# Optimization experiments

Measured on AMD Instinct MI355X. Metric: run time of the kernel, lower is better.

Reference implementation:

```python
import jax, jax.numpy as jnp
import numpy as np
import math

D = 1024
L = 4096
B = 4

def setup_inputs() -> dict:
    key = jax.random.key(0)
    ks = jax.random.split(key, 6)
    x = jax.random.normal(ks[0], (B, L, D), dtype=jnp.float32)
    base_phases = jax.random.normal(ks[1], (L, D), dtype=jnp.float32) * math.pi
    s = 1.0 / math.sqrt(D)
    W_v = jax.random.normal(ks[2], (D, D), dtype=jnp.float32) * s
    b_v = jnp.zeros((D,), dtype=jnp.float32)
    ln_g = jnp.ones((D,), dtype=jnp.float32)
    ln_b = jnp.zeros((D,), dtype=jnp.float32)
    W_o = jax.random.normal(ks[3], (D, D), dtype=jnp.float32) * s
    b_o = jnp.zeros((D,), dtype=jnp.float32)
    return {"x": x, "base_phases": base_phases, "W_v": W_v, "b_v": b_v,
            "ln_g": ln_g, "ln_b": ln_b, "W_o": W_o, "b_o": b_o}

def _layernorm(x, g, b, eps=1e-5):
    mu = jnp.mean(x, axis=-1, keepdims=True)
    var = jnp.mean(jnp.square(x - mu), axis=-1, keepdims=True)
    return (x - mu) * jax.lax.rsqrt(var + eps) * g + b

def reference(x, base_phases, W_v, b_v, ln_g, ln_b, W_o, b_o):
    Bv, Lv, Dv = x.shape
    phases = base_phases[:Lv][None, :, :]          # [1, L, D]
    cosp, sinp = jnp.cos(phases), jnp.sin(phases)
    value = jnp.einsum('bld,ed->ble', x, W_v) + b_v  # Linear(D,D)
    mem_real = jnp.cumsum(value * cosp, axis=1)
    mem_imag = jnp.cumsum(value * sinp, axis=1)
    retrieved = (mem_real * cosp + mem_imag * sinp) / math.sqrt(Dv)
    out = jnp.einsum('bld,ed->ble', _layernorm(retrieved, ln_g, ln_b), W_o) + b_o
    return x + out
```

## Files before the change

### kernel.cpp

```cpp
#include <hip/hip_runtime.h>
#include <stdint.h>


#define D_DIM 1024
#define L_DIM 4096
#define B_DIM 4
#define M_DIM (B_DIM * L_DIM)
#define CHUNK 64
#define NCH (L_DIM / CHUNK)
#define NT 16

typedef __attribute__((ext_vector_type(8))) short short8;
typedef __attribute__((ext_vector_type(4))) float f32x4;

__device__ __forceinline__ float bf2f(uint32_t h) {
  union { uint32_t u; float f; } x; x.u = h << 16; return x.f;
}
__device__ __forceinline__ uint16_t f2bf(float f) {
  union { float f; uint32_t u; } x; x.f = f;
  uint32_t u = x.u;
  u += 0x7fffu + ((u >> 16) & 1u);
  return (uint16_t)(u >> 16);
}

__global__ void k_prep(const float* __restrict__ x, const float* __restrict__ Wv,
                       const float* __restrict__ Wo, const float* __restrict__ g,
                       const float* __restrict__ bln, const float* __restrict__ bo,
                       uint16_t* __restrict__ xb, uint16_t* __restrict__ wv,
                       uint16_t* __restrict__ wob, float* __restrict__ u,
                       float* __restrict__ vb) {
  int blk = blockIdx.x;
  int tid = threadIdx.x;
  if (blk < 8192 + 512) {
    const float* in = (blk < 8192) ? x : Wv;
    uint16_t* outp = (blk < 8192) ? xb : wv;
    int base = (blk < 8192) ? blk : (blk - 8192);
    int i = (base * 256 + tid) * 8;
    float4 a = *(const float4*)(in + i);
    float4 b = *(const float4*)(in + i + 4);
    ushort4 o0 = { f2bf(a.x), f2bf(a.y), f2bf(a.z), f2bf(a.w) };
    ushort4 o1 = { f2bf(b.x), f2bf(b.y), f2bf(b.z), f2bf(b.w) };
    *(ushort4*)(outp + i) = o0;
    *(ushort4*)(outp + i + 4) = o1;
    return;
  }
  int e = blk - 8704;
  int d = tid * 4;
  float4 w  = *(const float4*)(Wo + (size_t)e * D_DIM + d);
  float4 gg = *(const float4*)(g + d);
  float4 bb = *(const float4*)(bln + d);
  float gw0 = gg.x * w.x, gw1 = gg.y * w.y, gw2 = gg.z * w.z, gw3 = gg.w * w.w;
  ushort4 o = { f2bf(gw0), f2bf(gw1), f2bf(gw2), f2bf(gw3) };
  *(ushort4*)(wob + (size_t)e * D_DIM + d) = o;
  float su = gw0 + gw1 + gw2 + gw3;
  float sv = bb.x * w.x + bb.y * w.y + bb.z * w.z + bb.w * w.w;
#pragma unroll
  for (int off = 32; off > 0; off >>= 1) {
    su += __shfl_down(su, off);
    sv += __shfl_down(sv, off);
  }
  __shared__ float s1[4], s2[4];
  int wid = tid >> 6, lane = tid & 63;
  if (lane == 0) { s1[wid] = su; s2[wid] = sv; }
  __syncthreads();
  if (tid == 0) {
    u[e]  = s1[0] + s1[1] + s1[2] + s1[3];
    vb[e] = s2[0] + s2[1] + s2[2] + s2[3] + bo[e];
  }
}

template <int MODE>
__global__ __launch_bounds__(512, 2) void k_gemm(
    const uint16_t* __restrict__ A, const uint16_t* __restrict__ W,
    void* __restrict__ outp,
    const float* __restrict__ p0, const float* __restrict__ p1,
    const float* __restrict__ mu, const float* __restrict__ inv,
    const uint16_t* __restrict__ xres) {
  __shared__ char lds[8 * 16384];
  const int tid = threadIdx.x;
  const int lane = tid & 63;
  const int wid = tid >> 6;
  const int wm = wid >> 2;
  const int wn = wid & 3;

  const int idx = blockIdx.x;
  const int bm = (idx & 7) * 8 + ((idx >> 3) >> 2);
  const int bn = (idx >> 3) & 3;

  const int srow = tid >> 3;
  const int scb  = (tid & 7) * 16;
  const int scbs = scb ^ ((srow & 7) << 4);

#define GLL(SRC, DST)                                                            \
  __builtin_amdgcn_global_load_lds((const __attribute__((address_space(1))) void*)(SRC), \
                                   (__attribute__((address_space(3))) void*)(DST), 16, 0, 0)

#define STAGE_A(KS, HA)                                                          \
  do {                                                                           \
    char* _d = lds + ((((KS)&1) * 4 + (HA)) << 14) + tid * 16;                   \
    const char* _s = (const char*)A +                                            \
        (size_t)(bm * 256 + (HA) * 128 + srow) * 2048 + (KS) * 128 + scbs;       \
    GLL(_s, _d);                                                                 \
    GLL(_s + (size_t)64 * 2048, _d + 8192);                                      \
  } while (0)

#define STAGE_B(KS, HB)                                                          \
  do {                                                                           \
    char* _d = lds + ((((KS)&1) * 4 + 2 + (HB)) << 14) + tid * 16;               \
    const char* _s = (const char*)W +                                            \
        (size_t)(bn * 256 + (HB) * 128 + srow) * 2048 + (KS) * 128 + scbs;       \
    GLL(_s, _d);                                                                 \
    GLL(_s + (size_t)64 * 2048, _d + 8192);                                      \
  } while (0)

  const int axor = (lane & 7) << 4;
  const int afr  = lane & 15;
  const int acol = (lane >> 4) * 16;

#define LD_A(PAR, I, KK)                                                         \
  (*(const short8*)(lds + (((PAR) * 4 + wm) << 14) + ((I) * 16 + afr) * 128 +    \
                    (((KK) * 64 + acol) ^ axor)))
#define LD_B(PAR, J, KK)                                                         \
  (*(const short8*)(lds + (((PAR) * 4 + 2 + (wn >> 1)) << 14) +                  \
                    ((wn & 1) * 64 + (J) * 16 + afr) * 128 +                     \
                    (((KK) * 64 + acol) ^ axor)))

#define MFMA(AV, BV, CV) __builtin_amdgcn_mfma_f32_16x16x32_bf16(AV, BV, CV, 0, 0, 0)
#define SB0() __builtin_amdgcn_sched_barrier(0)

  f32x4 acc[8][4];
#pragma unroll
  for (int i = 0; i < 8; ++i)
#pragma unroll
    for (int j = 0; j < 4; ++j)
      acc[i][j] = (f32x4){0.f, 0.f, 0.f, 0.f};

  STAGE_A(0, 0); STAGE_A(0, 1);
  STAGE_B(0, 0); STAGE_B(0, 1);
  asm volatile("s_waitcnt vmcnt(0)" ::: "memory");
  __builtin_amdgcn_s_barrier();

  for (int ks = 0; ks < NT; ++ks) {
    const int par = ks & 1;
    short8 Af0, Af1, Af2, Af3, Bf0, Bf1, Bf2, Bf3;

    Bf0 = LD_B(par, 0, 0); Bf1 = LD_B(par, 1, 0); Bf2 = LD_B(par, 2, 0); Bf3 = LD_B(par, 3, 0);
    Af0 = LD_A(par, 0, 0); Af1 = LD_A(par, 1, 0); Af2 = LD_A(par, 2, 0); Af3 = LD_A(par, 3, 0);
    SB0();
    if (ks + 1 < NT) { STAGE_A(ks + 1, 0); STAGE_A(ks + 1, 1); }
    __builtin_amdgcn_s_barrier();
    asm volatile("s_waitcnt lgkmcnt(0)" ::: "memory");
    SB0();
    __builtin_amdgcn_s_setprio(1);
#pragma unroll
    for (int j = 0; j < 4; ++j) {
      const short8 bj = (j == 0) ? Bf0 : (j == 1) ? Bf1 : (j == 2) ? Bf2 : Bf3;
      acc[0][j] = MFMA(Af0, bj, acc[0][j]);
      acc[1][j] = MFMA(Af1, bj, acc[1][j]);
      acc[2][j] = MFMA(Af2, bj, acc[2][j]);
      acc[3][j] = MFMA(Af3, bj, acc[3][j]);
    }
    __builtin_amdgcn_s_setprio(0);
    __builtin_amdgcn_s_barrier();

    Af0 = LD_A(par, 4, 0); Af1 = LD_A(par, 5, 0); Af2 = LD_A(par, 6, 0); Af3 = LD_A(par, 7, 0);
    SB0();
    if (ks + 1 < NT) { STAGE_B(ks + 1, 0); STAGE_B(ks + 1, 1); }
    __builtin_amdgcn_s_barrier();
    asm volatile("s_waitcnt lgkmcnt(0)" ::: "memory");
    SB0();
    __builtin_amdgcn_s_setprio(1);
#pragma unroll
    for (int j = 0; j < 4; ++j) {
      const short8 bj = (j == 0) ? Bf0 : (j == 1) ? Bf1 : (j == 2) ? Bf2 : Bf3;
      acc[4][j] = MFMA(Af0, bj, acc[4][j]);
      acc[5][j] = MFMA(Af1, bj, acc[5][j]);
      acc[6][j] = MFMA(Af2, bj, acc[6][j]);
      acc[7][j] = MFMA(Af3, bj, acc[7][j]);
    }
    __builtin_amdgcn_s_setprio(0);
    __builtin_amdgcn_s_barrier();

    Bf0 = LD_B(par, 0, 1); Bf1 = LD_B(par, 1, 1); Bf2 = LD_B(par, 2, 1); Bf3 = LD_B(par, 3, 1);
    Af0 = LD_A(par, 0, 1); Af1 = LD_A(par, 1, 1); Af2 = LD_A(par, 2, 1); Af3 = LD_A(par, 3, 1);
    SB0();
    __builtin_amdgcn_s_barrier();
    asm volatile("s_waitcnt lgkmcnt(0)" ::: "memory");
    SB0();
    __builtin_amdgcn_s_setprio(1);
#pragma unroll
    for (int j = 0; j < 4; ++j) {
      const short8 bj = (j == 0) ? Bf0 : (j == 1) ? Bf1 : (j == 2) ? Bf2 : Bf3;
      acc[0][j] = MFMA(Af0, bj, acc[0][j]);
      acc[1][j] = MFMA(Af1, bj, acc[1][j]);
      acc[2][j] = MFMA(Af2, bj, acc[2][j]);
      acc[3][j] = MFMA(Af3, bj, acc[3][j]);
    }
    __builtin_amdgcn_s_setprio(0);
    asm volatile("s_waitcnt vmcnt(4)" ::: "memory");
    __builtin_amdgcn_s_barrier();

    Af0 = LD_A(par, 4, 1); Af1 = LD_A(par, 5, 1); Af2 = LD_A(par, 6, 1); Af3 = LD_A(par, 7, 1);
    SB0();
    __builtin_amdgcn_s_barrier();
    asm volatile("s_waitcnt lgkmcnt(0)" ::: "memory");
    SB0();
    __builtin_amdgcn_s_setprio(1);
#pragma unroll
    for (int j = 0; j < 4; ++j) {
      const short8 bj = (j == 0) ? Bf0 : (j == 1) ? Bf1 : (j == 2) ? Bf2 : Bf3;
      acc[4][j] = MFMA(Af0, bj, acc[4][j]);
      acc[5][j] = MFMA(Af1, bj, acc[5][j]);
      acc[6][j] = MFMA(Af2, bj, acc[6][j]);
      acc[7][j] = MFMA(Af3, bj, acc[7][j]);
    }
    __builtin_amdgcn_s_setprio(0);
    asm volatile("s_waitcnt vmcnt(0)" ::: "memory");
    __builtin_amdgcn_s_barrier();
  }

  if (MODE == 0) {
    uint16_t* outv = (uint16_t*)outp;
    __syncthreads();
#pragma unroll
    for (int i = 0; i < 8; ++i)
#pragma unroll
      for (int r = 0; r < 4; ++r) {
        int row = wm * 128 + i * 16 + (lane >> 4) * 4 + r;
#pragma unroll
        for (int j = 0; j < 4; ++j) {
          int ncol = wn * 64 + j * 16 + (lane & 15);
          float v = acc[i][j][r] + p0[bn * 256 + ncol];
          *(uint16_t*)(lds + row * 512 + ((ncol * 2) ^ ((row & 7) << 4))) = f2bf(v);
        }
      }
    __syncthreads();
    {
      int row = tid >> 1, half = tid & 1;
      uint16_t* gdst = outv + (size_t)(bm * 256 + row) * D_DIM + bn * 256 + half * 128;
#pragma unroll
      for (int s = 0; s < 16; ++s) {
        short8 v = *(const short8*)(lds + row * 512 +
                                    ((half * 256 + s * 16) ^ ((row & 7) << 4)));
        *(short8*)(gdst + s * 8) = v;
      }
    }
  } else {
    float* outf = (float*)outp;
#pragma unroll
    for (int i = 0; i < 8; ++i)
#pragma unroll
      for (int r = 0; r < 4; ++r) {
        int m = bm * 256 + wm * 128 + i * 16 + (lane >> 4) * 4 + r;
        float im = inv[m], mm = mu[m];
#pragma unroll
        for (int j = 0; j < 4; ++j) {
          int n = bn * 256 + wn * 64 + j * 16 + (lane & 15);
          outf[(size_t)m * D_DIM + n] =
              im * acc[i][j][r] - im * mm * p0[n] + p1[n] +
              bf2f(xres[(size_t)m * D_DIM + n]);
        }
      }
  }
#undef GLL
#undef STAGE_A
#undef STAGE_B
#undef LD_A
#undef LD_B
#undef MFMA
#undef SB0
}

__global__ void k_passA(const uint16_t* __restrict__ value, const float* __restrict__ phases,
                        float* __restrict__ pr, float* __restrict__ pi) {
  int d0 = blockIdx.x * 512 + threadIdx.x * 2;
  int c = blockIdx.y, b = blockIdx.z;
  const uint16_t* vp = value + ((size_t)(b * L_DIM + c * CHUNK)) * D_DIM + d0;
  const float* pp = phases + (size_t)(c * CHUNK) * D_DIM + d0;
  float sr0 = 0, si0 = 0, sr1 = 0, si1 = 0;
#pragma unroll 4
  for (int l = 0; l < CHUNK; ++l) {
    uint32_t vv = *(const uint32_t*)vp; vp += D_DIM;
    float2 ph = *(const float2*)pp; pp += D_DIM;
    float v0 = bf2f(vv & 0xffffu), v1 = bf2f(vv >> 16);
    float s0, c0, s1, c1;
    __sincosf(ph.x, &s0, &c0);
    __sincosf(ph.y, &s1, &c1);
    sr0 += v0 * c0; si0 += v0 * s0;
    sr1 += v1 * c1; si1 += v1 * s1;
  }
  size_t o = ((size_t)b * NCH + c) * D_DIM + d0;
  *(float2*)(pr + o) = make_float2(sr0, sr1);
  *(float2*)(pi + o) = make_float2(si0, si1);
}

__global__ void k_passB(float* __restrict__ pr, float* __restrict__ pi) {
  int d = blockIdx.x * 256 + threadIdx.x;
  int b = blockIdx.y;
  size_t base = (size_t)b * NCH * D_DIM + d;
  float r[NCH], im[NCH];
#pragma unroll
  for (int c = 0; c < NCH; ++c) r[c] = pr[base + (size_t)c * D_DIM];
#pragma unroll
  for (int c = 0; c < NCH; ++c) im[c] = pi[base + (size_t)c * D_DIM];
  float rr = 0, ri = 0;
#pragma unroll
  for (int c = 0; c < NCH; ++c) {
    float t = r[c]; r[c] = rr; rr += t;
    t = im[c]; im[c] = ri; ri += t;
  }
#pragma unroll
  for (int c = 0; c < NCH; ++c) pr[base + (size_t)c * D_DIM] = r[c];
#pragma unroll
  for (int c = 0; c < NCH; ++c) pi[base + (size_t)c * D_DIM] = im[c];
}

__global__ void k_passC(const uint16_t* __restrict__ value, const float* __restrict__ phases,
                        const float* __restrict__ pr, const float* __restrict__ pi,
                        uint16_t* __restrict__ ret) {
  int d0 = blockIdx.x * 512 + threadIdx.x * 2;
  int c = blockIdx.y, b = blockIdx.z;
  size_t o = ((size_t)b * NCH + c) * D_DIM + d0;
  float2 r0 = *(const float2*)(pr + o);
  float2 i0 = *(const float2*)(pi + o);
  float mr0 = r0.x, mr1 = r0.y, mi0 = i0.x, mi1 = i0.y;
  size_t rowoff = ((size_t)(b * L_DIM + c * CHUNK)) * D_DIM + d0;
  const uint16_t* vp = value + rowoff;
  uint16_t* rp = ret + rowoff;
  const float* pp = phases + (size_t)(c * CHUNK) * D_DIM + d0;
  const float isd = 0.03125f;
#pragma unroll 4
  for (int l = 0; l < CHUNK; ++l) {
    uint32_t vv = *(const uint32_t*)vp; vp += D_DIM;
    float2 ph = *(const float2*)pp; pp += D_DIM;
    float v0 = bf2f(vv & 0xffffu), v1 = bf2f(vv >> 16);
    float s0, c0, s1, c1;
    __sincosf(ph.x, &s0, &c0);
    __sincosf(ph.y, &s1, &c1);
    mr0 += v0 * c0; mi0 += v0 * s0;
    mr1 += v1 * c1; mi1 += v1 * s1;
    float o0 = (mr0 * c0 + mi0 * s0) * isd;
    float o1 = (mr1 * c1 + mi1 * s1) * isd;
    *(uint32_t*)rp = (uint32_t)f2bf(o0) | ((uint32_t)f2bf(o1) << 16);
    rp += D_DIM;
  }
}

__global__ void k_stats(const uint16_t* __restrict__ ret, float* __restrict__ mu,
                        float* __restrict__ inv) {
  int m = blockIdx.x, tid = threadIdx.x;
  ushort4 v = *(const ushort4*)(ret + (size_t)m * D_DIM + tid * 4);
  float f0 = bf2f(v.x), f1 = bf2f(v.y), f2_ = bf2f(v.z), f3 = bf2f(v.w);
  float s = f0 + f1 + f2_ + f3;
  float ss = f0 * f0 + f1 * f1 + f2_ * f2_ + f3 * f3;
#pragma unroll
  for (int off = 32; off > 0; off >>= 1) {
    s += __shfl_down(s, off);
    ss += __shfl_down(ss, off);
  }
  __shared__ float a1[4], a2[4];
  int wid = tid >> 6, lane = tid & 63;
  if (lane == 0) { a1[wid] = s; a2[wid] = ss; }
  __syncthreads();
  if (tid == 0) {
    float S = a1[0] + a1[1] + a1[2] + a1[3];
    float SS = a2[0] + a2[1] + a2[2] + a2[3];
    float mm = S * (1.0f / 1024.0f);
    float var = SS * (1.0f / 1024.0f) - mm * mm;
    mu[m] = mm;
    inv[m] = rsqrtf(var + 1e-5f);
  }
}

extern "C" void kernel_launch(void* const* d_in, const int* in_sizes, int n_in,
                              void* d_out, int out_size, void* d_ws, size_t ws_size,
                              hipStream_t stream) {
  const float* x      = (const float*)d_in[0];
  const float* phases = (const float*)d_in[1];
  const float* Wv     = (const float*)d_in[2];
  const float* bv     = (const float*)d_in[3];
  const float* lng    = (const float*)d_in[4];
  const float* lnb    = (const float*)d_in[5];
  const float* Wo     = (const float*)d_in[6];
  const float* bo     = (const float*)d_in[7];
  float* out = (float*)d_out;

  char* ws = (char*)d_ws;
  uint16_t* xb    = (uint16_t*)(ws);
  uint16_t* value = (uint16_t*)(ws + (32ull << 20));
  uint16_t* wv    = (uint16_t*)(ws + (64ull << 20));
  uint16_t* wob   = (uint16_t*)(ws + (66ull << 20));
  float* pr       = (float*)(ws + (68ull << 20));
  float* pi       = (float*)(ws + (69ull << 20));
  float* u        = (float*)(ws + (70ull << 20));
  float* vb       = (float*)(ws + (70ull << 20) + 4096);
  float* mu       = (float*)(ws + (71ull << 20));
  float* inv      = (float*)(ws + (72ull << 20));
  uint16_t* retr  = value;

  k_prep<<<8192 + 512 + 1024, 256, 0, stream>>>(x, Wv, Wo, lng, lnb, bo,
                                                xb, wv, wob, u, vb);
  k_gemm<0><<<(M_DIM / 256) * (D_DIM / 256), 512, 0, stream>>>(
      xb, wv, value, bv, nullptr, nullptr, nullptr, nullptr);
  k_passA<<<dim3(2, NCH, B_DIM), 256, 0, stream>>>(value, phases, pr, pi);
  k_passB<<<dim3(D_DIM / 256, B_DIM), 256, 0, stream>>>(pr, pi);
  k_passC<<<dim3(2, NCH, B_DIM), 256, 0, stream>>>(value, phases, pr, pi, retr);
  k_stats<<<M_DIM, 256, 0, stream>>>(retr, mu, inv);
  k_gemm<1><<<(M_DIM / 256) * (D_DIM / 256), 512, 0, stream>>>(
      retr, wob, out, u, vb, mu, inv, xb);
}
```

Before: 149.6 us.

## Fuse fp32-to-bf16 conversion of x into first GEMM's A-tile loading

Removes the separate pass that converted x to a bf16 copy. The first GEMM now loads fp32 x tiles into registers, converts them to bf16 and writes them into swizzled LDS between MFMA phases. The residual add in the output GEMM reads fp32 x directly instead of the bf16 copy, which also slightly improves accuracy. This removes a 64MB read plus 32MB write plus 32MB reread of x, at the cost of double the A-tile global bytes in GEMM0, more registers, and losing the asynchronous global-to-LDS path for A.

```diff
diff --git a/kernel.cpp b/kernel.cpp
--- a/kernel.cpp
+++ b/kernel.cpp
@@ -22,29 +22,28 @@
   u += 0x7fffu + ((u >> 16) & 1u);
   return (uint16_t)(u >> 16);
 }
-
-__global__ void k_prep(const float* __restrict__ x, const float* __restrict__ Wv,
-                       const float* __restrict__ Wo, const float* __restrict__ g,
-                       const float* __restrict__ bln, const float* __restrict__ bo,
-                       uint16_t* __restrict__ xb, uint16_t* __restrict__ wv,
+__device__ __forceinline__ uint32_t pk2(float lo, float hi) {
+  return (uint32_t)f2bf(lo) | ((uint32_t)f2bf(hi) << 16);
+}
+
+__global__ void k_prep(const float* __restrict__ Wv, const float* __restrict__ Wo,
+                       const float* __restrict__ g, const float* __restrict__ bln,
+                       const float* __restrict__ bo, uint16_t* __restrict__ wv,
                        uint16_t* __restrict__ wob, float* __restrict__ u,
                        float* __restrict__ vb) {
   int blk = blockIdx.x;
   int tid = threadIdx.x;
-  if (blk < 8192 + 512) {
-    const float* in = (blk < 8192) ? x : Wv;
-    uint16_t* outp = (blk < 8192) ? xb : wv;
-    int base = (blk < 8192) ? blk : (blk - 8192);
-    int i = (base * 256 + tid) * 8;
-    float4 a = *(const float4*)(in + i);
-    float4 b = *(const float4*)(in + i + 4);
+  if (blk < 512) {
+    int i = (blk * 256 + tid) * 8;
+    float4 a = *(const float4*)(Wv + i);
+    float4 b = *(const float4*)(Wv + i + 4);
     ushort4 o0 = { f2bf(a.x), f2bf(a.y), f2bf(a.z), f2bf(a.w) };
     ushort4 o1 = { f2bf(b.x), f2bf(b.y), f2bf(b.z), f2bf(b.w) };
-    *(ushort4*)(outp + i) = o0;
-    *(ushort4*)(outp + i + 4) = o1;
+    *(ushort4*)(wv + i) = o0;
+    *(ushort4*)(wv + i + 4) = o1;
     return;
   }
-  int e = blk - 8704;
+  int e = blk - 512;
   int d = tid * 4;
   float4 w  = *(const float4*)(Wo + (size_t)e * D_DIM + d);
   float4 gg = *(const float4*)(g + d);
@@ -75,7 +74,7 @@
     void* __restrict__ outp,
     const float* __restrict__ p0, const float* __restrict__ p1,
     const float* __restrict__ mu, const float* __restrict__ inv,
-    const uint16_t* __restrict__ xres) {
+    const float* __restrict__ xres, const float* __restrict__ Af32) {
   __shared__ char lds[8 * 16384];
   const int tid = threadIdx.x;
   const int lane = tid & 63;
@@ -90,6 +89,11 @@
   const int srow = tid >> 3;
   const int scb  = (tid & 7) * 16;
   const int scbs = scb ^ ((srow & 7) << 4);
+
+  const int arow = tid >> 2;
+  const int acf  = (tid & 3) * 16;
+  const int acb  = (tid & 3) * 32;
+  const int aswz = (arow & 7) << 4;
 
 #define GLL(SRC, DST)                                                            \
   __builtin_amdgcn_global_load_lds((const __attribute__((address_space(1))) void*)(SRC), \
@@ -113,6 +117,33 @@
     GLL(_s + (size_t)64 * 2048, _d + 8192);                                      \
   } while (0)
 
+#define A_ISSUE(KS, HA, R)                                                       \
+  do {                                                                           \
+    const float* _s = Af32 + (size_t)(bm * 256 + (HA) * 128 + arow) * D_DIM +    \
+                      (KS) * 64 + acf;                                           \
+    R[0] = *(const float4*)(_s);      R[1] = *(const float4*)(_s + 4);           \
+    R[2] = *(const float4*)(_s + 8);  R[3] = *(const float4*)(_s + 12);          \
+  } while (0)
+
+#define CVT_WRITE(KSP, R0, R1)                                                   \
+  do {                                                                           \
+    char* _d0 = lds + (((KSP) * 4 + 0) << 14) + arow * 128;                      \
+    char* _d1 = lds + (((KSP) * 4 + 1) << 14) + arow * 128;                      \
+    int4 _g;                                                                     \
+    _g.x = pk2(R0[0].x, R0[0].y); _g.y = pk2(R0[0].z, R0[0].w);                  \
+    _g.z = pk2(R0[1].x, R0[1].y); _g.w = pk2(R0[1].z, R0[1].w);                  \
+    *(int4*)(_d0 + (acb ^ aswz)) = _g;                                           \
+    _g.x = pk2(R0[2].x, R0[2].y); _g.y = pk2(R0[2].z, R0[2].w);                  \
+    _g.z = pk2(R0[3].x, R0[3].y); _g.w = pk2(R0[3].z, R0[3].w);                  \
+    *(int4*)(_d0 + ((acb + 16) ^ aswz)) = _g;                                    \
+    _g.x = pk2(R1[0].x, R1[0].y); _g.y = pk2(R1[0].z, R1[0].w);                  \
+    _g.z = pk2(R1[1].x, R1[1].y); _g.w = pk2(R1[1].z, R1[1].w);                  \
+    *(int4*)(_d1 + (acb ^ aswz)) = _g;                                           \
+    _g.x = pk2(R1[2].x, R1[2].y); _g.y = pk2(R1[2].z, R1[2].w);                  \
+    _g.z = pk2(R1[3].x, R1[3].y); _g.w = pk2(R1[3].z, R1[3].w);                  \
+    *(int4*)(_d1 + ((acb + 16) ^ aswz)) = _g;                                    \
+  } while (0)
+
   const int axor = (lane & 7) << 4;
   const int afr  = lane & 15;
   const int acol = (lane >> 4) * 16;
@@ -135,19 +166,32 @@
     for (int j = 0; j < 4; ++j)
       acc[i][j] = (f32x4){0.f, 0.f, 0.f, 0.f};
 
-  STAGE_A(0, 0); STAGE_A(0, 1);
-  STAGE_B(0, 0); STAGE_B(0, 1);
-  asm volatile("s_waitcnt vmcnt(0)" ::: "memory");
+  if constexpr (MODE == 0) {
+    float4 q0[4], q1[4];
+    A_ISSUE(0, 0, q0); A_ISSUE(0, 1, q1);
+    STAGE_B(0, 0); STAGE_B(0, 1);
+    CVT_WRITE(0, q0, q1);
+    asm volatile("s_waitcnt vmcnt(0)" ::: "memory");
+    asm volatile("s_waitcnt lgkmcnt(0)" ::: "memory");
+  } else {
+    STAGE_A(0, 0); STAGE_A(0, 1);
+    STAGE_B(0, 0); STAGE_B(0, 1);
+    asm volatile("s_waitcnt vmcnt(0)" ::: "memory");
+  }
   __builtin_amdgcn_s_barrier();
 
   for (int ks = 0; ks < NT; ++ks) {
     const int par = ks & 1;
     short8 Af0, Af1, Af2, Af3, Bf0, Bf1, Bf2, Bf3;
+    float4 rA0[4], rA1[4];
 
     Bf0 = LD_B(par, 0, 0); Bf1 = LD_B(par, 1, 0); Bf2 = LD_B(par, 2, 0); Bf3 = LD_B(par, 3, 0);
     Af0 = LD_A(par, 0, 0); Af1 = LD_A(par, 1, 0); Af2 = LD_A(par, 2, 0); Af3 = LD_A(par, 3, 0);
     SB0();
-    if (ks + 1 < NT) { STAGE_A(ks + 1, 0); STAGE_A(ks + 1, 1); }
+    if (ks + 1 < NT) {
+      if constexpr (MODE == 0) { A_ISSUE(ks + 1, 0, rA0); A_ISSUE(ks + 1, 1, rA1); }
+      else                     { STAGE_A(ks + 1, 0); STAGE_A(ks + 1, 1); }
+    }
     __builtin_amdgcn_s_barrier();
     asm volatile("s_waitcnt lgkmcnt(0)" ::: "memory");
     SB0();
@@ -184,6 +228,9 @@
     Bf0 = LD_B(par, 0, 1); Bf1 = LD_B(par, 1, 1); Bf2 = LD_B(par, 2, 1); Bf3 = LD_B(par, 3, 1);
     Af0 = LD_A(par, 0, 1); Af1 = LD_A(par, 1, 1); Af2 = LD_A(par, 2, 1); Af3 = LD_A(par, 3, 1);
     SB0();
+    if constexpr (MODE == 0) {
+      if (ks + 1 < NT) CVT_WRITE((ks + 1) & 1, rA0, rA1);
+    }
     __builtin_amdgcn_s_barrier();
     asm volatile("s_waitcnt lgkmcnt(0)" ::: "memory");
     SB0();
@@ -197,7 +244,9 @@
       acc[3][j] = MFMA(Af3, bj, acc[3][j]);
     }
     __builtin_amdgcn_s_setprio(0);
-    asm volatile("s_waitcnt vmcnt(4)" ::: "memory");
+    if constexpr (MODE == 1) {
+      asm volatile("s_waitcnt vmcnt(4)" ::: "memory");
+    }
     __builtin_amdgcn_s_barrier();
 
     Af0 = LD_A(par, 4, 1); Af1 = LD_A(par, 5, 1); Af2 = LD_A(par, 6, 1); Af3 = LD_A(par, 7, 1);
@@ -258,13 +307,15 @@
           int n = bn * 256 + wn * 64 + j * 16 + (lane & 15);
           outf[(size_t)m * D_DIM + n] =
               im * acc[i][j][r] - im * mm * p0[n] + p1[n] +
-              bf2f(xres[(size_t)m * D_DIM + n]);
+              xres[(size_t)m * D_DIM + n];
         }
       }
   }
 #undef GLL
 #undef STAGE_A
 #undef STAGE_B
+#undef A_ISSUE
+#undef CVT_WRITE
 #undef LD_A
 #undef LD_B
 #undef MFMA
@@ -386,26 +437,24 @@
   float* out = (float*)d_out;
 
   char* ws = (char*)d_ws;
-  uint16_t* xb    = (uint16_t*)(ws);
-  uint16_t* value = (uint16_t*)(ws + (32ull << 20));
-  uint16_t* wv    = (uint16_t*)(ws + (64ull << 20));
-  uint16_t* wob   = (uint16_t*)(ws + (66ull << 20));
-  float* pr       = (float*)(ws + (68ull << 20));
-  float* pi       = (float*)(ws + (69ull << 20));
-  float* u        = (float*)(ws + (70ull << 20));
-  float* vb       = (float*)(ws + (70ull << 20) + 4096);
-  float* mu       = (float*)(ws + (71ull << 20));
-  float* inv      = (float*)(ws + (72ull << 20));
+  uint16_t* value = (uint16_t*)(ws);
+  uint16_t* wv    = (uint16_t*)(ws + (32ull << 20));
+  uint16_t* wob   = (uint16_t*)(ws + (34ull << 20));
+  float* pr       = (float*)(ws + (36ull << 20));
+  float* pi       = (float*)(ws + (37ull << 20));
+  float* u        = (float*)(ws + (38ull << 20));
+  float* vb       = (float*)(ws + (38ull << 20) + 4096);
+  float* mu       = (float*)(ws + (39ull << 20));
+  float* inv      = (float*)(ws + (40ull << 20));
   uint16_t* retr  = value;
 
-  k_prep<<<8192 + 512 + 1024, 256, 0, stream>>>(x, Wv, Wo, lng, lnb, bo,
-                                                xb, wv, wob, u, vb);
+  k_prep<<<512 + 1024, 256, 0, stream>>>(Wv, Wo, lng, lnb, bo, wv, wob, u, vb);
   k_gemm<0><<<(M_DIM / 256) * (D_DIM / 256), 512, 0, stream>>>(
-      xb, wv, value, bv, nullptr, nullptr, nullptr, nullptr);
+      nullptr, wv, value, bv, nullptr, nullptr, nullptr, nullptr, x);
   k_passA<<<dim3(2, NCH, B_DIM), 256, 0, stream>>>(value, phases, pr, pi);
   k_passB<<<dim3(D_DIM / 256, B_DIM), 256, 0, stream>>>(pr, pi);
   k_passC<<<dim3(2, NCH, B_DIM), 256, 0, stream>>>(value, phases, pr, pi, retr);
   k_stats<<<M_DIM, 256, 0, stream>>>(retr, mu, inv);
   k_gemm<1><<<(M_DIM / 256) * (D_DIM / 256), 512, 0, stream>>>(
-      retr, wob, out, u, vb, mu, inv, xb);
-}
+      retr, wob, out, u, vb, mu, inv, x, nullptr);
+}
```

New measurement: 161.7 us. +8.1%, slower.
